# Kernel tuning notes

Hardware: AMD Instinct MI355X
Metric: run time of the kernel (lower is better)

Reference implementation:

```python
import jax, jax.numpy as jnp
import numpy as np

NUM_HEADS = 8
EPS = 1e-12  # torch F.normalize eps


def setup_inputs() -> dict:
    key = jax.random.key(0)
    k1, k2, k3 = jax.random.split(key, 3)
    b, c, h, w = 4, 384, 128, 128
    x = jax.random.normal(k1, (b, c, h, w), dtype=jnp.float32)
    qkv_w = jax.random.normal(k2, (3 * c, c), dtype=jnp.float32) * (1.0 / np.sqrt(c))
    proj_w = jax.random.normal(k3, (c, c), dtype=jnp.float32) * (1.0 / np.sqrt(c))
    temperature = jnp.ones((NUM_HEADS, 1, 1), dtype=jnp.float32)
    return {"x": x, "qkv_w": qkv_w, "proj_w": proj_w, "temperature": temperature}


def _l2_normalize(t):
    # matches torch F.normalize(dim=-1): t / max(||t||_2, eps)
    n = jnp.sqrt(jnp.sum(t * t, axis=-1, keepdims=True))
    return t / jnp.maximum(n, EPS)


def reference(x, qkv_w, proj_w, temperature):
    b, c, h, w = x.shape
    heads = NUM_HEADS
    ch = c // heads  # per-head channel dim
    n = h * w
    # 1x1 conv == channel matmul
    qkv = jnp.einsum('bchw,oc->bohw', x, qkv_w)          # [b, 3c, h, w]
    qkv = qkv.reshape(b, 3, heads, ch, n)                # split qkv / heads / flatten spatial
    q, k, v = qkv[:, 0], qkv[:, 1], qkv[:, 2]            # [b, heads, ch, n]
    q = _l2_normalize(q)
    k = _l2_normalize(k)
    attn = jnp.einsum('bhcn,bhdn->bhcd', q, k) * temperature  # [b, heads, ch, ch]
    attn = jax.nn.softmax(attn, axis=-1)
    out = jnp.einsum('bhcd,bhdn->bhcn', attn, v)         # [b, heads, ch, n]
    out = out.reshape(b, c, h, w)
    out = jnp.einsum('bchw,oc->bohw', out, proj_w)       # 1x1 projection
    return out
```

## Files before the change

kernel.cpp:

```cpp
#include <hip/hip_runtime.h>
#include <stdint.h>

#define HW 16384
#define CH 384
#define NS 32

typedef float  f32x4  __attribute__((ext_vector_type(4)));
typedef short  short8 __attribute__((ext_vector_type(8)));
typedef __bf16 bf16x8 __attribute__((ext_vector_type(8)));
typedef unsigned short u16;
typedef u16 u16x4 __attribute__((ext_vector_type(4)));

__device__ __forceinline__ u16 f2bf(float f) {
  union { float f; uint32_t u; } v; v.f = f;
  uint32_t r = v.u + 0x7fffu + ((v.u >> 16) & 1u);
  return (u16)(r >> 16);
}
__device__ __forceinline__ float bf2f(u16 v) {
  union { uint32_t u; float f; } x; x.u = ((uint32_t)v) << 16; return x.f;
}
__device__ __forceinline__ f32x4 zero4() { f32x4 z = {0.f, 0.f, 0.f, 0.f}; return z; }

__device__ __forceinline__ f32x4 mfma_bf16(short8 a, short8 b, f32x4 c) {
  return __builtin_amdgcn_mfma_f32_16x16x32_bf16(
      __builtin_bit_cast(bf16x8, a), __builtin_bit_cast(bf16x8, b), c, 0, 0, 0);
}

__device__ __forceinline__ void gload16(const void* g, void* lds) {
  auto gp = (const __attribute__((address_space(1))) uint32_t*)(uintptr_t)g;
  auto lp = (__attribute__((address_space(3))) uint32_t*)(uintptr_t)lds;
  __builtin_amdgcn_global_load_lds(gp, lp, 16, 0, 0);
}

__global__ __launch_bounds__(256) void k_prep(const float* __restrict__ w,
                                              u16* __restrict__ wbf,
                                              u16* __restrict__ wvt) {
  __shared__ u16 tl[64][66];
  const int bid = blockIdx.x, t = threadIdx.x;
  if (bid < 1728) {
    const int i = bid * 256 + t;
    wbf[i] = f2bf(w[i]);
    return;
  }
  const int q = bid - 1728;
  const int ci = q % 6, di = q / 6;
#pragma unroll
  for (int jj = 0; jj < 4; ++jj) {
    const int r = (t >> 4) + jj * 16;
    f32x4 v = *(const f32x4*)(w + (size_t)(768 + di * 64 + r) * CH + ci * 64 + (t & 15) * 4);
#pragma unroll
    for (int i = 0; i < 4; ++i) tl[(t & 15) * 4 + i][r] = f2bf(v[i]);
  }
  __syncthreads();
#pragma unroll
  for (int jj = 0; jj < 2; ++jj) {
    const int c = (t >> 3) + jj * 32;
    short8 v = *(const short8*)(&tl[c][(t & 7) * 8]);
    *(short8*)(wvt + (size_t)(ci * 64 + c) * CH + di * 64 + (t & 7) * 8) = v;
  }
}

__global__ __launch_bounds__(256) void k_transpose_x(const float* __restrict__ x,
                                                     u16* __restrict__ xT,
                                                     u16* __restrict__ xb) {
  __shared__ u16 tile[64][66];
  const int b = blockIdx.z, c0 = blockIdx.y * 64, n0 = blockIdx.x * 64;
  const int t = threadIdx.x;
  const float* xp = x + (size_t)b * CH * HW;
  u16* xbp = xb + (size_t)b * CH * HW;
  const int nq = t & 15;
  const int cr = t >> 4;
#pragma unroll
  for (int jj = 0; jj < 4; ++jj) {
    const int c = cr + jj * 16;
    f32x4 v = *(const f32x4*)(xp + (size_t)(c0 + c) * HW + n0 + nq * 4);
    u16x4 pk;
#pragma unroll
    for (int i = 0; i < 4; ++i) { u16 bv = f2bf(v[i]); tile[nq * 4 + i][c] = bv; pk[i] = bv; }
    *(u16x4*)(xbp + (size_t)(c0 + c) * HW + n0 + nq * 4) = pk;
  }
  __syncthreads();
  u16* xtb = xT + (size_t)b * HW * CH;
  const int cc = t & 7;
  const int r0 = t >> 3;
#pragma unroll
  for (int jj = 0; jj < 2; ++jj) {
    const int r = r0 + jj * 32;
    short8 v = *(const short8*)(&tile[r][cc * 8]);
    *(short8*)(xtb + (size_t)(n0 + r) * CH + c0 + cc * 8) = v;
  }
}

template <int STRIDE>
__device__ __forceinline__ void stageS(u16* lds, const u16* __restrict__ g, int t) {
  const int w = t >> 6;
#pragma unroll
  for (int s = 0; s < 2; ++s) {
    const int r = s * 32 + (t >> 3);
    const int g8 = (t & 7) ^ (r & 7);
    const int gr = 2 * r + (g8 >> 2);
    gload16(g + (size_t)gr * STRIDE + (g8 & 3) * 8, lds + s * 2048 + w * 512);
  }
}

__global__ __launch_bounds__(256) void k_gramx(const u16* __restrict__ xb,
                                               float* __restrict__ part) {
  const int orig = blockIdx.x;
  const int L = (orig & 7) * (6 * NS * 4 / 8) + (orig >> 3);
  const int pair = L % 6;
  const int ns = (L / 6) % NS;
  const int b = L / (6 * NS);
  const int i = pair < 3 ? 0 : (pair < 5 ? 1 : 2);
  const int j = pair < 3 ? pair : (pair < 5 ? pair - 2 : 2);
  const int t = threadIdx.x, lane = t & 63, w = t >> 6;
  const int wo = w & 1, wn = w >> 1;
  const u16* pa = xb + ((size_t)b * CH + i * 128) * HW + ns * 512;
  const u16* pb = xb + ((size_t)b * CH + j * 128) * HW + ns * 512;

  __shared__ u16 As[3][64 * 64];
  __shared__ u16 Bs[3][64 * 64];

  f32x4 acc[4][4];
#pragma unroll
  for (int a = 0; a < 4; ++a)
#pragma unroll
    for (int c = 0; c < 4; ++c) acc[a][c] = zero4();

#pragma unroll
  for (int p = 0; p < 2; ++p) {
    stageS<HW>(As[p], pa + p * 32, t);
    stageS<HW>(Bs[p], pb + p * 32, t);
  }
  const int ks = lane >> 4;
  for (int kt = 0; kt < 16; ++kt) {
    if (kt < 15) asm volatile("s_waitcnt vmcnt(4)" ::: "memory");
    else         asm volatile("s_waitcnt vmcnt(0)" ::: "memory");
    asm volatile("s_barrier" ::: "memory");
    if (kt <= 13) {
      stageS<HW>(As[(kt + 2) % 3], pa + (kt + 2) * 32, t);
      stageS<HW>(Bs[(kt + 2) % 3], pb + (kt + 2) * 32, t);
    }
    const u16* Ac = As[kt % 3];
    const u16* Bc = Bs[kt % 3];
    short8 af[4], bf[4];
#pragma unroll
    for (int mi = 0; mi < 4; ++mi) {
      const int gr = wo * 64 + mi * 16 + (lane & 15);
      const int r = gr >> 1;
      const int p = ((gr & 1) * 4 + ks) ^ (r & 7);
      af[mi] = *(const short8*)(Ac + r * 64 + p * 8);
    }
#pragma unroll
    for (int ni = 0; ni < 4; ++ni) {
      const int gr = wn * 64 + ni * 16 + (lane & 15);
      const int r = gr >> 1;
      const int p = ((gr & 1) * 4 + ks) ^ (r & 7);
      bf[ni] = *(const short8*)(Bc + r * 64 + p * 8);
    }
#pragma unroll
    for (int ni = 0; ni < 4; ++ni)
#pragma unroll
      for (int mi = 0; mi < 4; ++mi)
        acc[ni][mi] = mfma_bf16(bf[ni], af[mi], acc[ni][mi]);
  }
  float* dst = part + ((size_t)(b * 6 + pair) * NS + ns) * 16384;
#pragma unroll
  for (int ni = 0; ni < 4; ++ni)
#pragma unroll
    for (int mi = 0; mi < 4; ++mi) {
      const int ai = wo * 64 + mi * 16 + (lane & 15);
      const int bj = wn * 64 + ni * 16 + ((lane >> 4) << 2);
      *(f32x4*)(dst + (size_t)ai * 128 + bj) = acc[ni][mi];
    }
}

__global__ __launch_bounds__(256) void k_greduce(const float* __restrict__ part,
                                                 u16* __restrict__ Goff,
                                                 float* __restrict__ Gd) {
  const int cq = blockIdx.x, pair = blockIdx.y, b = blockIdx.z;
  const int i = pair < 3 ? 0 : (pair < 5 ? 1 : 2);
  const int j = pair < 3 ? pair : (pair < 5 ? pair - 2 : 2);
  const int t = threadIdx.x;
  const int c0 = cq * 16;
  __shared__ u16 tl[16][136];
  const float* src = part + (size_t)(b * 6 + pair) * NS * 16384;
#pragma unroll
  for (int p = 0; p < 2; ++p) {
    const int q = t + p * 256;
    const int ai = q >> 2;
    const int bj = c0 + (q & 3) * 4;
    f32x4 s = zero4();
    for (int ns = 0; ns < NS; ++ns) s += *(const f32x4*)(src + (size_t)ns * 16384 + ai * 128 + bj);
    if (i == j) {
#pragma unroll
      for (int jj = 0; jj < 4; ++jj)
        if (ai == bj + jj) { Gd[b * CH + i * 128 + ai] = s[jj]; s[jj] = 0.f; }
    }
    u16x4 pk;
#pragma unroll
    for (int jj = 0; jj < 4; ++jj) { pk[jj] = f2bf(s[jj]); tl[bj - c0 + jj][ai] = pk[jj]; }
    *(u16x4*)(Goff + ((size_t)b * CH + i * 128 + ai) * CH + j * 128 + bj) = pk;
  }
  if (i != j) {
    __syncthreads();
    const int r = t >> 4;
    const int ch = (t & 15) * 8;
    short8 v = *(const short8*)(&tl[r][ch]);
    *(short8*)(Goff + ((size_t)b * CH + j * 128 + c0 + r) * CH + i * 128 + ch) = v;
  }
}

template <int TM>
__global__ __launch_bounds__(256) void k_mini(const u16* __restrict__ A,
                                              const u16* __restrict__ B,
                                              float* __restrict__ Tout,
                                              u16* __restrict__ Bout,
                                              const float* __restrict__ Gd,
                                              const u16* __restrict__ Wd) {
  const int nt = blockIdx.x, mt = blockIdx.y, b = blockIdx.z;
  __shared__ u16 Ws[4][64 * 64];
  __shared__ u16 Xs[4][64 * 64];
  const int t = threadIdx.x, lane = t & 63, w = t >> 6;
  const int wo = w & 1, wn = w >> 1;
  const u16* Ab = A + (TM ? 0 : (size_t)b * CH * CH) + (size_t)mt * 128 * CH;
  const u16* Bb = B + (TM ? (size_t)b * CH * CH : 0) + (size_t)nt * 128 * CH;

  f32x4 acc[4][4];
#pragma unroll
  for (int a = 0; a < 4; ++a)
#pragma unroll
    for (int c = 0; c < 4; ++c) acc[a][c] = zero4();

#pragma unroll
  for (int p = 0; p < 3; ++p) {
    stageS<CH>(Ws[p], Ab + p * 32, t);
    stageS<CH>(Xs[p], Bb + p * 32, t);
  }
  const int ks = lane >> 4;
  for (int kt = 0; kt < 12; ++kt) {
    if (kt <= 9)       asm volatile("s_waitcnt vmcnt(8)" ::: "memory");
    else if (kt == 10) asm volatile("s_waitcnt vmcnt(4)" ::: "memory");
    else               asm volatile("s_waitcnt vmcnt(0)" ::: "memory");
    asm volatile("s_barrier" ::: "memory");
    if (kt < 9) {
      stageS<CH>(Ws[(kt + 3) & 3], Ab + (kt + 3) * 32, t);
      stageS<CH>(Xs[(kt + 3) & 3], Bb + (kt + 3) * 32, t);
    }
    const u16* Wc = Ws[kt & 3];
    const u16* Xc = Xs[kt & 3];
    short8 af[4], bfr[4];
#pragma unroll
    for (int mi = 0; mi < 4; ++mi) {
      const int gr = wo * 64 + mi * 16 + (lane & 15);
      const int r = gr >> 1;
      const int p = ((gr & 1) * 4 + ks) ^ (r & 7);
      af[mi] = *(const short8*)(Wc + r * 64 + p * 8);
    }
#pragma unroll
    for (int ni = 0; ni < 4; ++ni) {
      const int gr = wn * 64 + ni * 16 + (lane & 15);
      const int r = gr >> 1;
      const int p = ((gr & 1) * 4 + ks) ^ (r & 7);
      bfr[ni] = *(const short8*)(Xc + r * 64 + p * 8);
    }
#pragma unroll
    for (int ni = 0; ni < 4; ++ni)
#pragma unroll
      for (int mi = 0; mi < 4; ++mi)
        acc[ni][mi] = mfma_bf16(bfr[ni], af[mi], acc[ni][mi]);
  }

#pragma unroll
  for (int ni = 0; ni < 4; ++ni)
#pragma unroll
    for (int mi = 0; mi < 4; ++mi) {
      const int tr = mt * 128 + wo * 64 + mi * 16 + (lane & 15);
      const int d0 = nt * 128 + wn * 64 + ni * 16 + ((lane >> 4) << 2);
      if (TM) {
        f32x4 g = *(const f32x4*)(Gd + b * CH + d0);
        u16x4 w4 = *(const u16x4*)(Wd + (size_t)tr * CH + d0);
        f32x4 v;
#pragma unroll
        for (int jj = 0; jj < 4; ++jj) v[jj] = acc[ni][mi][jj] + bf2f(w4[jj]) * g[jj];
        *(f32x4*)(Tout + ((size_t)b * 768 + tr) * CH + d0) = v;
      } else {
        u16x4 pk;
#pragma unroll
        for (int jj = 0; jj < 4; ++jj) pk[jj] = f2bf(acc[ni][mi][jj]);
        *(u16x4*)(Bout + ((size_t)b * CH + tr) * CH + d0) = pk;
      }
    }
}

__global__ __launch_bounds__(384) void k_attn(const float* __restrict__ T,
                                              const u16* __restrict__ wbf,
                                              const float* __restrict__ projw,
                                              const float* __restrict__ temp,
                                              u16* __restrict__ Mbf) {
  const int h = blockIdx.x, b = blockIdx.y, t = threadIdx.x;
  __shared__ float Sl[48][48];
  __shared__ float attn[48][48];
  __shared__ float nrm[96];
  const float* T1 = T + ((size_t)b * 768 + h * 48) * CH;
  const float* T2 = T1 + (size_t)384 * CH;
  const u16* wk = wbf + (size_t)(384 + h * 48) * CH;

  if (t < 64) {
    const int lane = t;
    f32x4 sa[3][3];
#pragma unroll
    for (int a = 0; a < 3; ++a)
#pragma unroll
      for (int c = 0; c < 3; ++c) sa[a][c] = zero4();
    for (int kk = 0; kk < 12; ++kk) {
      const int kc = kk * 32 + ((lane >> 4) << 3);
      short8 afr[3], bfr[3];
#pragma unroll
      for (int mi = 0; mi < 3; ++mi) {
        const float* s = T1 + (size_t)(mi * 16 + (lane & 15)) * CH + kc;
        f32x4 v0 = *(const f32x4*)(s);
        f32x4 v1 = *(const f32x4*)(s + 4);
        short8 a;
#pragma unroll
        for (int jj = 0; jj < 4; ++jj) { a[jj] = (short)f2bf(v0[jj]); a[4 + jj] = (short)f2bf(v1[jj]); }
        afr[mi] = a;
      }
#pragma unroll
      for (int ni = 0; ni < 3; ++ni)
        bfr[ni] = *(const short8*)(wk + (size_t)(ni * 16 + (lane & 15)) * CH + kc);
#pragma unroll
      for (int ni = 0; ni < 3; ++ni)
#pragma unroll
        for (int mi = 0; mi < 3; ++mi)
          sa[ni][mi] = mfma_bf16(bfr[ni], afr[mi], sa[ni][mi]);
    }
#pragma unroll
    for (int ni = 0; ni < 3; ++ni)
#pragma unroll
      for (int mi = 0; mi < 3; ++mi)
#pragma unroll
        for (int jj = 0; jj < 4; ++jj)
          Sl[mi * 16 + (lane & 15)][ni * 16 + ((lane >> 4) << 2) + jj] = sa[ni][mi][jj];
  } else if (t < 160) {
    const int r = t - 64;
    const float* Tr = (r < 48) ? T1 + (size_t)r * CH : T2 + (size_t)(r - 48) * CH;
    const u16* wr = (r < 48) ? wbf + (size_t)(h * 48 + r) * CH
                             : wbf + (size_t)(384 + h * 48 + (r - 48)) * CH;
    float a = 0.f;
    for (int c4 = 0; c4 < 96; ++c4) {
      f32x4 tv = *(const f32x4*)(Tr + c4 * 4);
      u16x4 wv = *(const u16x4*)(wr + c4 * 4);
#pragma unroll
      for (int jj = 0; jj < 4; ++jj) a = fmaf(tv[jj], bf2f(wv[jj]), a);
    }
    nrm[r] = a;
  }
  __syncthreads();
  if (t < 48) {
    const float th = temp[h];
    const float inq = 1.f / fmaxf(sqrtf(nrm[t]), 1e-12f);
    float l[48];
    float mx = -3.4e38f;
#pragma unroll
    for (int u = 0; u < 48; ++u) {
      float ik = 1.f / fmaxf(sqrtf(nrm[48 + u]), 1e-12f);
      float lg = Sl[t][u] * inq * ik * th;
      l[u] = lg;
      mx = fmaxf(mx, lg);
    }
    float sum = 0.f;
#pragma unroll
    for (int u = 0; u < 48; ++u) { float e = __expf(l[u] - mx); l[u] = e; sum += e; }
    float inv = 1.f / sum;
#pragma unroll
    for (int u = 0; u < 48; ++u) attn[t][u] = l[u] * inv;
  }
  __syncthreads();
  float pw[48];
#pragma unroll
  for (int c = 0; c < 48; ++c) pw[c] = projw[(size_t)t * CH + h * 48 + c];
  u16* Mb = Mbf + ((size_t)b * CH + t) * CH + h * 48;
#pragma unroll 4
  for (int d = 0; d < 48; ++d) {
    float a = 0.f;
#pragma unroll
    for (int c = 0; c < 48; ++c) a = fmaf(pw[c], attn[c][d], a);
    Mb[d] = f2bf(a);
  }
}

__global__ __launch_bounds__(256) void k_final(const u16* __restrict__ P,
                                               const u16* __restrict__ Bx,
                                               float* __restrict__ outp) {
  constexpr int NWG = 3 * 128 * 4;
  constexpr int CHUNK = NWG / 8;
  const int orig = blockIdx.x;
  const int L = (orig & 7) * CHUNK + (orig >> 3);
  const int ot = L % 3;
  const int ntg = L / 3;
  const int b = ntg >> 7;
  const int nt = ntg & 127;

  __shared__ u16 Ws[4][64 * 64];
  __shared__ u16 Xs[4][64 * 64];
  const int t = threadIdx.x, lane = t & 63, w = t >> 6;
  const int wo = w & 1, wn = w >> 1;
  const u16* Ab = P + (size_t)b * CH * CH + (size_t)ot * 128 * CH;
  const u16* Bb = Bx + (size_t)b * HW * CH + (size_t)nt * 128 * CH;

  f32x4 acc[4][4];
#pragma unroll
  for (int a = 0; a < 4; ++a)
#pragma unroll
    for (int c = 0; c < 4; ++c) acc[a][c] = zero4();

#pragma unroll
  for (int p = 0; p < 3; ++p) {
    stageS<CH>(Ws[p], Ab + p * 32, t);
    stageS<CH>(Xs[p], Bb + p * 32, t);
  }
  const int ks = lane >> 4;
  for (int kt = 0; kt < 12; ++kt) {
    if (kt <= 9)       asm volatile("s_waitcnt vmcnt(8)" ::: "memory");
    else if (kt == 10) asm volatile("s_waitcnt vmcnt(4)" ::: "memory");
    else               asm volatile("s_waitcnt vmcnt(0)" ::: "memory");
    asm volatile("s_barrier" ::: "memory");
    if (kt < 9) {
      stageS<CH>(Ws[(kt + 3) & 3], Ab + (kt + 3) * 32, t);
      stageS<CH>(Xs[(kt + 3) & 3], Bb + (kt + 3) * 32, t);
    }
    const u16* Wc = Ws[kt & 3];
    const u16* Xc = Xs[kt & 3];
    short8 af[4], bfr[4];
#pragma unroll
    for (int mi = 0; mi < 4; ++mi) {
      const int gr = wo * 64 + mi * 16 + (lane & 15);
      const int r = gr >> 1;
      const int p = ((gr & 1) * 4 + ks) ^ (r & 7);
      af[mi] = *(const short8*)(Wc + r * 64 + p * 8);
    }
#pragma unroll
    for (int ni = 0; ni < 4; ++ni) {
      const int gr = wn * 64 + ni * 16 + (lane & 15);
      const int r = gr >> 1;
      const int p = ((gr & 1) * 4 + ks) ^ (r & 7);
      bfr[ni] = *(const short8*)(Xc + r * 64 + p * 8);
    }
#pragma unroll
    for (int ni = 0; ni < 4; ++ni)
#pragma unroll
      for (int mi = 0; mi < 4; ++mi)
        acc[ni][mi] = mfma_bf16(bfr[ni], af[mi], acc[ni][mi]);
  }
  float* ob = outp + (size_t)b * CH * HW;
#pragma unroll
  for (int ni = 0; ni < 4; ++ni)
#pragma unroll
    for (int mi = 0; mi < 4; ++mi) {
      int o = ot * 128 + wo * 64 + mi * 16 + (lane & 15);
      int n = nt * 128 + wn * 64 + ni * 16 + ((lane >> 4) << 2);
      *(f32x4*)(ob + (size_t)o * HW + n) = acc[ni][mi];
    }
}

extern "C" void kernel_launch(void* const* d_in, const int* in_sizes, int n_in,
                              void* d_out, int out_size, void* d_ws, size_t ws_size,
                              hipStream_t stream) {
  const float* x     = (const float*)d_in[0];
  const float* qkvw  = (const float*)d_in[1];
  const float* projw = (const float*)d_in[2];
  const float* temp  = (const float*)d_in[3];
  float* out = (float*)d_out;
  char* ws = (char*)d_ws;

  u16*   xT   = (u16*)(ws);
  u16*   wbf  = (u16*)(ws + 50331648);
  u16*   wvt  = (u16*)(ws + 51216384);
  u16*   Goff = (u16*)(ws + 51511296);
  float* Gd   = (float*)(ws + 52690944);
  float* Tf   = (float*)(ws + 52697088);
  u16*   Mbf  = (u16*)(ws + 57415680);
  u16*   Pbf  = (u16*)(ws + 58595328);
  u16*   xb   = (u16*)d_out;
  float* part = (float*)((char*)d_out + 50331648);

  k_prep<<<dim3(1764), 256, 0, stream>>>(qkvw, wbf, wvt);
  k_transpose_x<<<dim3(HW / 64, CH / 64, 4), 256, 0, stream>>>(x, xT, xb);
  k_gramx<<<dim3(6 * NS * 4), 256, 0, stream>>>(xb, part);
  k_greduce<<<dim3(8, 6, 4), 256, 0, stream>>>(part, Goff, Gd);
  k_mini<1><<<dim3(3, 6, 4), 256, 0, stream>>>(wbf, Goff, Tf, nullptr, Gd, wbf);
  k_attn<<<dim3(8, 4), 384, 0, stream>>>(Tf, wbf, projw, temp, Mbf);
  k_mini<0><<<dim3(3, 3, 4), 256, 0, stream>>>(Mbf, wvt, nullptr, Pbf, nullptr, nullptr);
  k_final<<<dim3(3 * 128 * 4), 256, 0, stream>>>(Pbf, xT, out);
}
```

Before: 158.0 us.

## Merge weight prep into x transpose, vectorize tile writes, shrink final GEMM pipeline

The weight conversion kernel and the x transpose/bf16 kernel become one launch, so the small weight work overlaps the large x pass and one launch disappears. The x transpose now has each thread handle 4 consecutive channels, letting it write the LDS tile with 4-wide vector stores instead of scalar ones. The final GEMM's LDS pipeline drops from 4 to 3 stages with launch_bounds(256,3), cutting shared memory so more workgroups fit per CU, at the cost of less prefetch depth.

After: 155.0 us (median of 3 runs). About the same (-1.9%).

```diff
diff --git a/kernel.cpp b/kernel.cpp
--- a/kernel.cpp
+++ b/kernel.cpp
@@ -32,52 +32,58 @@
   __builtin_amdgcn_global_load_lds(gp, lp, 16, 0, 0);
 }
 
-__global__ __launch_bounds__(256) void k_prep(const float* __restrict__ w,
-                                              u16* __restrict__ wbf,
-                                              u16* __restrict__ wvt) {
-  __shared__ u16 tl[64][66];
+__global__ __launch_bounds__(256) void k_prep_x(const float* __restrict__ x,
+                                                u16* __restrict__ xT,
+                                                u16* __restrict__ xb,
+                                                const float* __restrict__ w,
+                                                u16* __restrict__ wbf,
+                                                u16* __restrict__ wvt) {
+  __shared__ u16 tile[64][66];
   const int bid = blockIdx.x, t = threadIdx.x;
-  if (bid < 1728) {
-    const int i = bid * 256 + t;
-    wbf[i] = f2bf(w[i]);
+  if (bid >= 6144) {
+    if (bid < 7872) {
+      const int i = (bid - 6144) * 256 + t;
+      wbf[i] = f2bf(w[i]);
+      return;
+    }
+    const int q = bid - 7872;
+    const int ci = q % 6, di = q / 6;
+#pragma unroll
+    for (int jj = 0; jj < 4; ++jj) {
+      const int r = (t >> 4) + jj * 16;
+      f32x4 v = *(const f32x4*)(w + (size_t)(768 + di * 64 + r) * CH + ci * 64 + (t & 15) * 4);
+#pragma unroll
+      for (int i = 0; i < 4; ++i) tile[(t & 15) * 4 + i][r] = f2bf(v[i]);
+    }
+    __syncthreads();
+#pragma unroll
+    for (int jj = 0; jj < 2; ++jj) {
+      const int c = (t >> 3) + jj * 32;
+      short8 v = *(const short8*)(&tile[c][(t & 7) * 8]);
+      *(short8*)(wvt + (size_t)(ci * 64 + c) * CH + di * 64 + (t & 7) * 8) = v;
+    }
     return;
   }
-  const int q = bid - 1728;
-  const int ci = q % 6, di = q / 6;
-#pragma unroll
-  for (int jj = 0; jj < 4; ++jj) {
-    const int r = (t >> 4) + jj * 16;
-    f32x4 v = *(const f32x4*)(w + (size_t)(768 + di * 64 + r) * CH + ci * 64 + (t & 15) * 4);
-#pragma unroll
-    for (int i = 0; i < 4; ++i) tl[(t & 15) * 4 + i][r] = f2bf(v[i]);
-  }
-  __syncthreads();
-#pragma unroll
-  for (int jj = 0; jj < 2; ++jj) {
-    const int c = (t >> 3) + jj * 32;
-    short8 v = *(const short8*)(&tl[c][(t & 7) * 8]);
-    *(short8*)(wvt + (size_t)(ci * 64 + c) * CH + di * 64 + (t & 7) * 8) = v;
-  }
-}
-
-__global__ __launch_bounds__(256) void k_transpose_x(const float* __restrict__ x,
-                                                     u16* __restrict__ xT,
-                                                     u16* __restrict__ xb) {
-  __shared__ u16 tile[64][66];
-  const int b = blockIdx.z, c0 = blockIdx.y * 64, n0 = blockIdx.x * 64;
-  const int t = threadIdx.x;
+  const int nt = bid & 255, cq = (bid >> 8) % 6, b = bid / 1536;
+  const int c0 = cq * 64, n0 = nt * 64;
   const float* xp = x + (size_t)b * CH * HW;
   u16* xbp = xb + (size_t)b * CH * HW;
   const int nq = t & 15;
-  const int cr = t >> 4;
-#pragma unroll
-  for (int jj = 0; jj < 4; ++jj) {
-    const int c = cr + jj * 16;
-    f32x4 v = *(const f32x4*)(xp + (size_t)(c0 + c) * HW + n0 + nq * 4);
+  const int cg = t >> 4;
+  u16 bv[4][4];
+#pragma unroll
+  for (int i = 0; i < 4; ++i) {
+    const int c = c0 + cg * 4 + i;
+    f32x4 v = *(const f32x4*)(xp + (size_t)c * HW + n0 + nq * 4);
     u16x4 pk;
 #pragma unroll
-    for (int i = 0; i < 4; ++i) { u16 bv = f2bf(v[i]); tile[nq * 4 + i][c] = bv; pk[i] = bv; }
-    *(u16x4*)(xbp + (size_t)(c0 + c) * HW + n0 + nq * 4) = pk;
+    for (int j = 0; j < 4; ++j) { bv[i][j] = f2bf(v[j]); pk[j] = bv[i][j]; }
+    *(u16x4*)(xbp + (size_t)c * HW + n0 + nq * 4) = pk;
+  }
+#pragma unroll
+  for (int j = 0; j < 4; ++j) {
+    u16x4 row = {bv[0][j], bv[1][j], bv[2][j], bv[3][j]};
+    *(u16x4*)(&tile[nq * 4 + j][cg * 4]) = row;
   }
   __syncthreads();
   u16* xtb = xT + (size_t)b * HW * CH;
@@ -389,9 +395,9 @@
   }
 }
 
-__global__ __launch_bounds__(256) void k_final(const u16* __restrict__ P,
-                                               const u16* __restrict__ Bx,
-                                               float* __restrict__ outp) {
+__global__ __launch_bounds__(256, 3) void k_final(const u16* __restrict__ P,
+                                                  const u16* __restrict__ Bx,
+                                                  float* __restrict__ outp) {
   constexpr int NWG = 3 * 128 * 4;
   constexpr int CHUNK = NWG / 8;
   const int orig = blockIdx.x;
@@ -401,8 +407,8 @@
   const int b = ntg >> 7;
   const int nt = ntg & 127;
 
-  __shared__ u16 Ws[4][64 * 64];
-  __shared__ u16 Xs[4][64 * 64];
+  __shared__ u16 Ws[3][64 * 64];
+  __shared__ u16 Xs[3][64 * 64];
   const int t = threadIdx.x, lane = t & 63, w = t >> 6;
   const int wo = w & 1, wn = w >> 1;
   const u16* Ab = P + (size_t)b * CH * CH + (size_t)ot * 128 * CH;
@@ -415,22 +421,21 @@
     for (int c = 0; c < 4; ++c) acc[a][c] = zero4();
 
 #pragma unroll
-  for (int p = 0; p < 3; ++p) {
+  for (int p = 0; p < 2; ++p) {
     stageS<CH>(Ws[p], Ab + p * 32, t);
     stageS<CH>(Xs[p], Bb + p * 32, t);
   }
   const int ks = lane >> 4;
   for (int kt = 0; kt < 12; ++kt) {
-    if (kt <= 9)       asm volatile("s_waitcnt vmcnt(8)" ::: "memory");
-    else if (kt == 10) asm volatile("s_waitcnt vmcnt(4)" ::: "memory");
-    else               asm volatile("s_waitcnt vmcnt(0)" ::: "memory");
+    if (kt < 11) asm volatile("s_waitcnt vmcnt(4)" ::: "memory");
+    else         asm volatile("s_waitcnt vmcnt(0)" ::: "memory");
     asm volatile("s_barrier" ::: "memory");
-    if (kt < 9) {
-      stageS<CH>(Ws[(kt + 3) & 3], Ab + (kt + 3) * 32, t);
-      stageS<CH>(Xs[(kt + 3) & 3], Bb + (kt + 3) * 32, t);
-    }
-    const u16* Wc = Ws[kt & 3];
-    const u16* Xc = Xs[kt & 3];
+    if (kt <= 9) {
+      stageS<CH>(Ws[(kt + 2) % 3], Ab + (kt + 2) * 32, t);
+      stageS<CH>(Xs[(kt + 2) % 3], Bb + (kt + 2) * 32, t);
+    }
+    const u16* Wc = Ws[kt % 3];
+    const u16* Xc = Xs[kt % 3];
     short8 af[4], bfr[4];
 #pragma unroll
     for (int mi = 0; mi < 4; ++mi) {
@@ -484,8 +489,7 @@
   u16*   xb   = (u16*)d_out;
   float* part = (float*)((char*)d_out + 50331648);
 
-  k_prep<<<dim3(1764), 256, 0, stream>>>(qkvw, wbf, wvt);
-  k_transpose_x<<<dim3(HW / 64, CH / 64, 4), 256, 0, stream>>>(x, xT, xb);
+  k_prep_x<<<dim3(7908), 256, 0, stream>>>(x, xT, xb, qkvw, wbf, wvt);
   k_gramx<<<dim3(6 * NS * 4), 256, 0, stream>>>(xb, part);
   k_greduce<<<dim3(8, 6, 4), 256, 0, stream>>>(part, Goff, Gd);
   k_mini<1><<<dim3(3, 6, 4), 256, 0, stream>>>(wbf, Goff, Tf, nullptr, Gd, wbf);
```
